# Kernel optimization log

Hardware: AMD Instinct MI355X
Metric: run time of the kernel (lower is better)

Reference implementation:

```python
import jax, jax.numpy as jnp
import numpy as np
from jax import lax

B, N, C_IN, H, W = 256, 64, 3, 8, 8
CH = [32, 64, 128]   # cnn channels per stage
D = 128              # fc / gnn width
OUT = 5
BN_EPS = 1e-5


def setup_inputs() -> dict:
    key = jax.random.key(0)
    ks = jax.random.split(key, 24)
    x = jax.random.normal(ks[0], (B, N, C_IN, H, W), jnp.float32)
    # sparse symmetric communication graph, no self loops (GCNConv adds them)
    a = jax.random.uniform(ks[1], (B, N, N)) < 0.15
    a = jnp.logical_or(a, jnp.swapaxes(a, 1, 2)).astype(jnp.float32)
    gso = a * (1.0 - jnp.eye(N, dtype=jnp.float32))

    def lin(k, o, i):
        return (jax.random.normal(k, (o, i), jnp.float32) / np.sqrt(i)).astype(jnp.float32)

    def conv(k, o, i):
        return (jax.random.normal(k, (o, i, 3, 3), jnp.float32) / np.sqrt(i * 9)).astype(jnp.float32)

    inp = {
        'x': x, 'gso': gso,
        'w_c1': conv(ks[2], CH[0], C_IN), 'b_c1': jnp.zeros((CH[0],), jnp.float32),
        'g_bn1': jnp.ones((CH[0],), jnp.float32), 'be_bn1': jnp.zeros((CH[0],), jnp.float32),
        'w_c2': conv(ks[3], CH[1], CH[0]), 'b_c2': jnp.zeros((CH[1],), jnp.float32),
        'g_bn2': jnp.ones((CH[1],), jnp.float32), 'be_bn2': jnp.zeros((CH[1],), jnp.float32),
        'w_c3': conv(ks[4], CH[2], CH[1]), 'b_c3': jnp.zeros((CH[2],), jnp.float32),
        'g_bn3': jnp.ones((CH[2],), jnp.float32), 'be_bn3': jnp.zeros((CH[2],), jnp.float32),
        'w_fc': lin(ks[5], D, CH[2]), 'b_fc': jnp.zeros((D,), jnp.float32),
        'w_g1': lin(ks[6], D, D), 'b_g1': jnp.zeros((D,), jnp.float32),
        'w_g2': lin(ks[7], D, D), 'b_g2': jnp.zeros((D,), jnp.float32),
        'w_out': lin(ks[8], OUT, D), 'b_out': jnp.zeros((OUT,), jnp.float32),
    }
    return inp


def _cnn_block(h, w, b, g, be):
    h = lax.conv_general_dilated(h, w, (1, 1), 'SAME',
                                 dimension_numbers=('NCHW', 'OIHW', 'NCHW'))
    h = h + b[None, :, None, None]
    # eval-mode BatchNorm2d with running_mean=0, running_var=1
    h = h * (g / jnp.sqrt(1.0 + BN_EPS))[None, :, None, None] + be[None, :, None, None]
    h = jax.nn.relu(h)
    h = lax.reduce_window(h, -jnp.inf, lax.max, (1, 1, 2, 2), (1, 1, 2, 2), 'VALID')
    return h


def _forward(x, gso, w_c1, b_c1, g_bn1, be_bn1, w_c2, b_c2, g_bn2, be_bn2,
             w_c3, b_c3, g_bn3, be_bn3, w_fc, b_fc, w_g1, b_g1, w_g2, b_g2,
             w_out, b_out):
    b, n = x.shape[0], x.shape[1]
    h = x.reshape(b * n, x.shape[2], x.shape[3], x.shape[4])  # vectorize agents
    h = _cnn_block(h, w_c1, b_c1, g_bn1, be_bn1)
    h = _cnn_block(h, w_c2, b_c2, g_bn2, be_bn2)
    h = _cnn_block(h, w_c3, b_c3, g_bn3, be_bn3)          # [B*N, CH2, 1, 1]
    h = h.reshape(b * n, -1)
    h = jax.nn.relu(h @ w_fc.T + b_fc)                    # [B*N, D]
    feat = h.reshape(b, n, -1)
    # GCNConv: add self loops (weight 1), symmetric normalization
    a1 = gso + jnp.eye(n, dtype=gso.dtype)
    dinv = lax.rsqrt(a1.sum(-1))                          # deg >= 1
    ahat = dinv[:, :, None] * a1 * dinv[:, None, :]       # [B, N, N]
    hg = jax.nn.relu(jnp.einsum('bij,bjf->bif', ahat, feat @ w_g1.T) + b_g1)
    hg = jax.nn.relu(jnp.einsum('bij,bjf->bif', ahat, hg @ w_g2.T) + b_g2)
    actions = hg @ w_out.T + b_out                        # [B, N, OUT]
    return actions


def reference(x, gso, w_c1, b_c1, g_bn1, be_bn1, w_c2, b_c2, g_bn2, be_bn2,
              w_c3, b_c3, g_bn3, be_bn3, w_fc, b_fc, w_g1, b_g1, w_g2, b_g2,
              w_out, b_out):
    return _forward(x, gso, w_c1, b_c1, g_bn1, be_bn1, w_c2, b_c2, g_bn2, be_bn2,
                    w_c3, b_c3, g_bn3, be_bn3, w_fc, b_fc, w_g1, b_g1, w_g2, b_g2,
                    w_out, b_out)
```

## Files before the change

kernel.cpp:

```cpp
#include <hip/hip_runtime.h>
#include <math.h>


typedef __attribute__((ext_vector_type(8))) short bf16x8;
typedef __attribute__((ext_vector_type(4))) float f32x4;

__device__ __forceinline__ short f2bf(float f) {
  union { float f; unsigned u; } v; v.f = f;
  unsigned r = v.u + 0x7fffu + ((v.u >> 16) & 1u);
  return (short)(r >> 16);
}
__device__ __forceinline__ float bf2f(unsigned short u) {
  union { unsigned u; float f; } v; v.u = ((unsigned)u) << 16;
  return v.f;
}

__global__ __launch_bounds__(256) void pack_all(
    const float* __restrict__ w_c1, const float* __restrict__ w_c2,
    const float* __restrict__ w_c3, const float* __restrict__ w_fc,
    const float* __restrict__ w_g1, const float* __restrict__ w_g2,
    short* __restrict__ B1, short* __restrict__ B2, short* __restrict__ B3,
    short* __restrict__ Wfc, short* __restrict__ Wg1, short* __restrict__ Wg2) {
  int idx = blockIdx.x * 256 + threadIdx.x;
  if (idx < 2048) {
    int j = idx & 7, lane = (idx >> 3) & 63, f = idx >> 9;
    int nt = f >> 1, ksp = f & 1;
    int col = lane & 15, quad = lane >> 4;
    int k = ksp * 32 + quad * 8 + j;
    int t = k >> 2, ic = k & 3;
    int oc = nt * 16 + col;
    float v = (t < 9 && ic < 3) ? w_c1[(oc * 3 + ic) * 9 + t] : 0.0f;
    B1[idx] = f2bf(v);
  } else if (idx < 20480) {
    int i2 = idx - 2048;
    int j = i2 & 7, lane = (i2 >> 3) & 63, f = i2 >> 9;
    int nt = f / 9, t = f - nt * 9;
    int col = lane & 15, quad = lane >> 4;
    int oc = nt * 16 + col, ic = quad * 8 + j;
    B2[i2] = f2bf(w_c2[(oc * 32 + ic) * 9 + t]);
  } else if (idx < 94208) {
    int i3 = idx - 20480;
    int j = i3 & 7, lane = (i3 >> 3) & 63, f = i3 >> 9;
    int ng = f / 18, ks = f - ng * 18;
    int col = lane & 15, quad = lane >> 4;
    int oc = ng * 16 + col;
    int k = ks * 32 + quad * 8 + j;
    int t = k >> 6, ic = k & 63;
    B3[i3] = f2bf(w_c3[(oc * 64 + ic) * 9 + t]);
  } else if (idx < 110592) {
    int i = idx - 94208; Wfc[i] = f2bf(w_fc[i]);
  } else if (idx < 126976) {
    int i = idx - 110592; Wg1[i] = f2bf(w_g1[i]);
  } else if (idx < 143360) {
    int i = idx - 126976; Wg2[i] = f2bf(w_g2[i]);
  }
}

__global__ __launch_bounds__(256, 2) void conv_all(
    const float* __restrict__ x, const short* __restrict__ B1f,
    const short* __restrict__ B2f, const short* __restrict__ B3f,
    const float* __restrict__ b1, const float* __restrict__ g1,
    const float* __restrict__ e1, const float* __restrict__ b2,
    const float* __restrict__ g2, const float* __restrict__ e2,
    const float* __restrict__ b3, const float* __restrict__ g3,
    const float* __restrict__ e3, short* __restrict__ c3) {
  __shared__ short sFrame[16 * 400];
  __shared__ short sc1[16 * 512];
  __shared__ short sc2[16 * 256];
  const int tid = threadIdx.x;
  const int s0 = blockIdx.x * 16;
  const int lane = tid & 63, w = tid >> 6;
  const int col = lane & 15, quad = lane >> 4;
  const int m = lane & 15;

  for (int i = tid; i < 800; i += 256)
    *(uint4*)(sFrame + i * 8) = (uint4){0, 0, 0, 0};
  __syncthreads();
#pragma unroll
  for (int it = 0; it < 4; ++it) {
    int p = it * 256 + tid;
    int si = p >> 6, pix = p & 63;
    int y = pix >> 3, xx2 = pix & 7;
    const float* xb = x + (s0 + si) * 192 + pix;
    ushort4 o;
    o.x = (unsigned short)f2bf(xb[0]);
    o.y = (unsigned short)f2bf(xb[64]);
    o.z = (unsigned short)f2bf(xb[128]);
    o.w = 0;
    *(ushort4*)(sFrame + si * 400 + ((y + 1) * 10 + xx2 + 1) * 4) = o;
  }
  __syncthreads();

  {
    bf16x8 Bf[2][2];
#pragma unroll
    for (int nt = 0; nt < 2; ++nt)
#pragma unroll
      for (int ks = 0; ks < 2; ++ks)
        Bf[nt][ks] = *(const bf16x8*)(B1f + ((nt * 2 + ks) << 9) + lane * 8);
    float Abn[2], Cbn[2];
#pragma unroll
    for (int nt = 0; nt < 2; ++nt) {
      int oc = nt * 16 + col;
      float a = g1[oc] * rsqrtf(1.0f + 1e-5f);
      Abn[nt] = a;
      Cbn[nt] = fmaf(b1[oc], a, e1[oc]);
    }
    const int t0 = 2 * quad, t1 = t0 + 1;
    const int ky0 = t0 / 3, kx0 = t0 - 3 * (t0 / 3);
    const int ky1 = t1 / 3, kx1 = t1 - 3 * (t1 / 3);
    const int pl = m >> 2, sub = m & 3;
    const int dy = sub >> 1, dx = sub & 1;
    const uint2 z2 = {0u, 0u};
#pragma unroll
    for (int sl = 0; sl < 4; ++sl) {
      const int si = w * 4 + sl;
      const short* xb = sFrame + si * 400;
#pragma unroll
      for (int tile = 0; tile < 4; ++tile) {
        const int pi = tile * 4 + pl;
        const int py = pi >> 2, px = pi & 3;
        const int cy = 2 * py + dy, cx = 2 * px + dx;
        union { bf16x8 v; uint2 u[2]; } a0, a1;
        a0.u[0] = *(const uint2*)(xb + ((cy + ky0) * 10 + cx + kx0) * 4);
        a0.u[1] = *(const uint2*)(xb + ((cy + ky1) * 10 + cx + kx1) * 4);
        uint2 u8 = *(const uint2*)(xb + ((cy + 2) * 10 + cx + 2) * 4);
        a1.u[0] = (quad == 0) ? u8 : z2;
        a1.u[1] = z2;
        f32x4 acc0 = {0, 0, 0, 0}, acc1 = {0, 0, 0, 0};
        acc0 = __builtin_amdgcn_mfma_f32_16x16x32_bf16(a0.v, Bf[0][0], acc0, 0, 0, 0);
        acc0 = __builtin_amdgcn_mfma_f32_16x16x32_bf16(a1.v, Bf[0][1], acc0, 0, 0, 0);
        acc1 = __builtin_amdgcn_mfma_f32_16x16x32_bf16(a0.v, Bf[1][0], acc1, 0, 0, 0);
        acc1 = __builtin_amdgcn_mfma_f32_16x16x32_bf16(a1.v, Bf[1][1], acc1, 0, 0, 0);
        const int piq = tile * 4 + quad;
#pragma unroll
        for (int nt = 0; nt < 2; ++nt) {
          f32x4 acc = nt ? acc1 : acc0;
          float p0 = fmaf(acc[0], Abn[nt], Cbn[nt]);
          float p1 = fmaf(acc[1], Abn[nt], Cbn[nt]);
          float p2 = fmaf(acc[2], Abn[nt], Cbn[nt]);
          float p3 = fmaf(acc[3], Abn[nt], Cbn[nt]);
          float mx = fmaxf(fmaxf(fmaxf(p0, p1), fmaxf(p2, p3)), 0.0f);
          sc1[si * 512 + piq * 32 + nt * 16 + col] = f2bf(mx);
        }
      }
    }
  }
  __syncthreads();

  {
    bf16x8 Bf[4][9];
#pragma unroll
    for (int nt = 0; nt < 4; ++nt)
#pragma unroll
      for (int t = 0; t < 9; ++t)
        Bf[nt][t] = *(const bf16x8*)(B2f + ((nt * 9 + t) << 9) + lane * 8);
    float Abn[4], Cbn[4];
#pragma unroll
    for (int nt = 0; nt < 4; ++nt) {
      int oc = nt * 16 + col;
      float a = g2[oc] * rsqrtf(1.0f + 1e-5f);
      Abn[nt] = a;
      Cbn[nt] = fmaf(b2[oc], a, e2[oc]);
    }
    const int q2 = m >> 2, sub = m & 3;
    const int cy = 2 * (q2 >> 1) + (sub >> 1);
    const int cx = 2 * (q2 & 1) + (sub & 1);
    int off[9];
    bool valid[9];
#pragma unroll
    for (int t = 0; t < 9; ++t) {
      int ky = t / 3, kx = t - 3 * (t / 3);
      int yy = cy + ky - 1, xx = cx + kx - 1;
      valid[t] = ((unsigned)yy < 4u) && ((unsigned)xx < 4u);
      int yc = min(max(yy, 0), 3), xc = min(max(xx, 0), 3);
      off[t] = (yc * 4 + xc) * 32 + quad * 8;
    }
    const bf16x8 zf = {0, 0, 0, 0, 0, 0, 0, 0};
#pragma unroll
    for (int sl = 0; sl < 4; ++sl) {
      const int si = w * 4 + sl;
      const short* ib = sc1 + si * 512;
      f32x4 acc[4];
#pragma unroll
      for (int nt = 0; nt < 4; ++nt) acc[nt] = (f32x4){0, 0, 0, 0};
#pragma unroll
      for (int t = 0; t < 9; ++t) {
        bf16x8 a = *(const bf16x8*)(ib + off[t]);
        if (!valid[t]) a = zf;
#pragma unroll
        for (int nt = 0; nt < 4; ++nt)
          acc[nt] = __builtin_amdgcn_mfma_f32_16x16x32_bf16(a, Bf[nt][t], acc[nt], 0, 0, 0);
      }
#pragma unroll
      for (int nt = 0; nt < 4; ++nt) {
        float p0 = fmaf(acc[nt][0], Abn[nt], Cbn[nt]);
        float p1 = fmaf(acc[nt][1], Abn[nt], Cbn[nt]);
        float p2 = fmaf(acc[nt][2], Abn[nt], Cbn[nt]);
        float p3 = fmaf(acc[nt][3], Abn[nt], Cbn[nt]);
        float mx = fmaxf(fmaxf(fmaxf(p0, p1), fmaxf(p2, p3)), 0.0f);
        sc2[si * 256 + quad * 64 + nt * 16 + col] = f2bf(mx);
      }
    }
  }
  __syncthreads();

  {
    const int cp = m & 3, sl3 = m >> 2;
    const int cy = cp >> 1, cx = cp & 1;
    const short* ib = sc2 + (w * 4 + sl3) * 256;
    bf16x8 A[18];
    const bf16x8 zf = {0, 0, 0, 0, 0, 0, 0, 0};
#pragma unroll
    for (int ks = 0; ks < 18; ++ks) {
      int t = ks >> 1;
      int ky = t / 3, kx = t - 3 * (t / 3);
      int iy = cy + ky - 1, ix = cx + kx - 1;
      bool valid = ((unsigned)iy < 2u) && ((unsigned)ix < 2u);
      int iyc = min(max(iy, 0), 1), ixc = min(max(ix, 0), 1);
      bf16x8 a = *(const bf16x8*)(ib + (iyc * 2 + ixc) * 64 + (ks & 1) * 32 + quad * 8);
      A[ks] = valid ? a : zf;
    }
    f32x4 acc[8];
#pragma unroll
    for (int i = 0; i < 8; ++i) acc[i] = (f32x4){0, 0, 0, 0};
#pragma unroll
    for (int ng = 0; ng < 8; ++ng) {
#pragma unroll
      for (int ks = 0; ks < 18; ++ks) {
        bf16x8 b = *(const bf16x8*)(B3f + (((ng * 18 + ks) << 6) + lane) * 8);
        acc[ng] = __builtin_amdgcn_mfma_f32_16x16x32_bf16(A[ks], b, acc[ng], 0, 0, 0);
      }
    }
    const int sample = s0 + w * 4 + quad;
#pragma unroll
    for (int ng = 0; ng < 8; ++ng) {
      int oc = ng * 16 + col;
      float a = g3[oc] * rsqrtf(1.0f + 1e-5f);
      float cc = fmaf(b3[oc], a, e3[oc]);
      float p0 = fmaf(acc[ng][0], a, cc);
      float p1 = fmaf(acc[ng][1], a, cc);
      float p2 = fmaf(acc[ng][2], a, cc);
      float p3 = fmaf(acc[ng][3], a, cc);
      float mx = fmaxf(fmaxf(fmaxf(p0, p1), fmaxf(p2, p3)), 0.0f);
      c3[sample * 128 + oc] = f2bf(mx);
    }
  }
}

__global__ __launch_bounds__(512) void fused_dense(
    const short* __restrict__ c3, const float* __restrict__ gso,
    const short* __restrict__ Wfc, const short* __restrict__ Wg1,
    const short* __restrict__ Wg2, const float* __restrict__ b_fc,
    const float* __restrict__ b_g1, const float* __restrict__ b_g2,
    const float* __restrict__ w_o, const float* __restrict__ b_o,
    float* __restrict__ out) {
  __shared__ short sAct[64 * 136];
  __shared__ short sT[128 * 72];
  __shared__ short sAhat[64 * 72];
  __shared__ float sDinv[64];
  __shared__ float sWo[640];
  const int tid = threadIdx.x;
  const int b = blockIdx.x;
  float* sG = (float*)sT;
  for (int i = tid; i < 4096; i += 512) sG[i] = gso[b * 4096 + i];
  for (int i = tid; i < 640; i += 512) sWo[i] = w_o[i];
  __syncthreads();
  if (tid < 64) {
    float ssum = 1.0f;
    for (int j = 0; j < 64; ++j) ssum += sG[j * 64 + tid];
    sDinv[tid] = rsqrtf(ssum);
  }
  __syncthreads();
  for (int i = tid; i < 4096; i += 512) {
    int r = i >> 6, c = i & 63;
    float v = sDinv[r] * (sG[i] + (r == c ? 1.0f : 0.0f)) * sDinv[c];
    sAhat[r * 72 + c] = f2bf(v);
  }
  for (int i = tid; i < 1024; i += 512) {
    int r = i >> 4, seg = i & 15;
    *(bf16x8*)(sAct + r * 136 + seg * 8) =
        *(const bf16x8*)(c3 + (b * 64 + r) * 128 + seg * 8);
  }
  __syncthreads();
  const int lane = tid & 63, w8 = tid >> 6;
  const int rg = w8 >> 1, nh = w8 & 1;
  const int col = lane & 15, quad = lane >> 4;
  const int arow = (rg * 16 + col) * 136;
  const int crow0 = (rg * 16 + quad * 4) * 136;
  bf16x8 A[4];
  f32x4 acc[4];

#pragma unroll
  for (int ks = 0; ks < 4; ++ks)
    A[ks] = *(const bf16x8*)(sAct + arow + ks * 32 + quad * 8);
  __syncthreads();
#pragma unroll
  for (int i = 0; i < 4; ++i) acc[i] = (f32x4){0, 0, 0, 0};
#pragma unroll
  for (int ntl = 0; ntl < 4; ++ntl) {
    const int n = (nh * 4 + ntl) * 16 + col;
#pragma unroll
    for (int ks = 0; ks < 4; ++ks) {
      bf16x8 bb = *(const bf16x8*)(Wfc + n * 128 + ks * 32 + quad * 8);
      acc[ntl] = __builtin_amdgcn_mfma_f32_16x16x32_bf16(A[ks], bb, acc[ntl], 0, 0, 0);
    }
  }
#pragma unroll
  for (int ntl = 0; ntl < 4; ++ntl) {
    const int n = (nh * 4 + ntl) * 16 + col;
    const float bv = b_fc[n];
#pragma unroll
    for (int reg = 0; reg < 4; ++reg)
      sAct[crow0 + reg * 136 + n] = f2bf(fmaxf(acc[ntl][reg] + bv, 0.0f));
  }
  __syncthreads();

#pragma unroll
  for (int ks = 0; ks < 4; ++ks)
    A[ks] = *(const bf16x8*)(sAct + arow + ks * 32 + quad * 8);
#pragma unroll
  for (int i = 0; i < 4; ++i) acc[i] = (f32x4){0, 0, 0, 0};
#pragma unroll
  for (int ntl = 0; ntl < 4; ++ntl) {
    const int n = (nh * 4 + ntl) * 16 + col;
#pragma unroll
    for (int ks = 0; ks < 4; ++ks) {
      bf16x8 bb = *(const bf16x8*)(Wg1 + n * 128 + ks * 32 + quad * 8);
      acc[ntl] = __builtin_amdgcn_mfma_f32_16x16x32_bf16(A[ks], bb, acc[ntl], 0, 0, 0);
    }
  }
#pragma unroll
  for (int ntl = 0; ntl < 4; ++ntl) {
    const int n = (nh * 4 + ntl) * 16 + col;
    ushort4 pk;
    pk.x = (unsigned short)f2bf(acc[ntl][0]);
    pk.y = (unsigned short)f2bf(acc[ntl][1]);
    pk.z = (unsigned short)f2bf(acc[ntl][2]);
    pk.w = (unsigned short)f2bf(acc[ntl][3]);
    *(ushort4*)(sT + n * 72 + rg * 16 + quad * 4) = pk;
  }
  __syncthreads();

  bf16x8 Ah[2];
#pragma unroll
  for (int ks = 0; ks < 2; ++ks)
    Ah[ks] = *(const bf16x8*)(sAhat + (rg * 16 + col) * 72 + ks * 32 + quad * 8);
#pragma unroll
  for (int i = 0; i < 4; ++i) acc[i] = (f32x4){0, 0, 0, 0};
#pragma unroll
  for (int ntl = 0; ntl < 4; ++ntl) {
    const int n = (nh * 4 + ntl) * 16 + col;
#pragma unroll
    for (int ks = 0; ks < 2; ++ks) {
      bf16x8 bb = *(const bf16x8*)(sT + n * 72 + ks * 32 + quad * 8);
      acc[ntl] = __builtin_amdgcn_mfma_f32_16x16x32_bf16(Ah[ks], bb, acc[ntl], 0, 0, 0);
    }
  }
#pragma unroll
  for (int ntl = 0; ntl < 4; ++ntl) {
    const int n = (nh * 4 + ntl) * 16 + col;
    const float bv = b_g1[n];
#pragma unroll
    for (int reg = 0; reg < 4; ++reg)
      sAct[crow0 + reg * 136 + n] = f2bf(fmaxf(acc[ntl][reg] + bv, 0.0f));
  }
  __syncthreads();

#pragma unroll
  for (int ks = 0; ks < 4; ++ks)
    A[ks] = *(const bf16x8*)(sAct + arow + ks * 32 + quad * 8);
#pragma unroll
  for (int i = 0; i < 4; ++i) acc[i] = (f32x4){0, 0, 0, 0};
#pragma unroll
  for (int ntl = 0; ntl < 4; ++ntl) {
    const int n = (nh * 4 + ntl) * 16 + col;
#pragma unroll
    for (int ks = 0; ks < 4; ++ks) {
      bf16x8 bb = *(const bf16x8*)(Wg2 + n * 128 + ks * 32 + quad * 8);
      acc[ntl] = __builtin_amdgcn_mfma_f32_16x16x32_bf16(A[ks], bb, acc[ntl], 0, 0, 0);
    }
  }
#pragma unroll
  for (int ntl = 0; ntl < 4; ++ntl) {
    const int n = (nh * 4 + ntl) * 16 + col;
    ushort4 pk;
    pk.x = (unsigned short)f2bf(acc[ntl][0]);
    pk.y = (unsigned short)f2bf(acc[ntl][1]);
    pk.z = (unsigned short)f2bf(acc[ntl][2]);
    pk.w = (unsigned short)f2bf(acc[ntl][3]);
    *(ushort4*)(sT + n * 72 + rg * 16 + quad * 4) = pk;
  }
  __syncthreads();

#pragma unroll
  for (int i = 0; i < 4; ++i) acc[i] = (f32x4){0, 0, 0, 0};
#pragma unroll
  for (int ntl = 0; ntl < 4; ++ntl) {
    const int n = (nh * 4 + ntl) * 16 + col;
#pragma unroll
    for (int ks = 0; ks < 2; ++ks) {
      bf16x8 bb = *(const bf16x8*)(sT + n * 72 + ks * 32 + quad * 8);
      acc[ntl] = __builtin_amdgcn_mfma_f32_16x16x32_bf16(Ah[ks], bb, acc[ntl], 0, 0, 0);
    }
  }
#pragma unroll
  for (int ntl = 0; ntl < 4; ++ntl) {
    const int n = (nh * 4 + ntl) * 16 + col;
    const float bv = b_g2[n];
#pragma unroll
    for (int reg = 0; reg < 4; ++reg)
      sAct[crow0 + reg * 136 + n] = f2bf(fmaxf(acc[ntl][reg] + bv, 0.0f));
  }
  __syncthreads();

  if (tid < 320) {
    const int j = tid / 5, o = tid - 5 * j;
    float a0 = 0.0f;
#pragma unroll
    for (int k8 = 0; k8 < 16; ++k8) {
      union { bf16x8 v; unsigned short u[8]; } h;
      h.v = *(const bf16x8*)(sAct + j * 136 + k8 * 8);
#pragma unroll
      for (int jj = 0; jj < 8; ++jj)
        a0 = fmaf(bf2f(h.u[jj]), sWo[o * 128 + k8 * 8 + jj], a0);
    }
    out[(b * 64 + j) * 5 + o] = a0 + b_o[o];
  }
}

extern "C" void kernel_launch(void* const* d_in, const int* in_sizes, int n_in,
                              void* d_out, int out_size, void* d_ws, size_t ws_size,
                              hipStream_t stream) {
  const float* x    = (const float*)d_in[0];
  const float* gso  = (const float*)d_in[1];
  const float* w_c1 = (const float*)d_in[2];
  const float* b_c1 = (const float*)d_in[3];
  const float* g_b1 = (const float*)d_in[4];
  const float* e_b1 = (const float*)d_in[5];
  const float* w_c2 = (const float*)d_in[6];
  const float* b_c2 = (const float*)d_in[7];
  const float* g_b2 = (const float*)d_in[8];
  const float* e_b2 = (const float*)d_in[9];
  const float* w_c3 = (const float*)d_in[10];
  const float* b_c3 = (const float*)d_in[11];
  const float* g_b3 = (const float*)d_in[12];
  const float* e_b3 = (const float*)d_in[13];
  const float* w_fc = (const float*)d_in[14];
  const float* b_fc = (const float*)d_in[15];
  const float* w_g1 = (const float*)d_in[16];
  const float* b_g1 = (const float*)d_in[17];
  const float* w_g2 = (const float*)d_in[18];
  const float* b_g2 = (const float*)d_in[19];
  const float* w_o  = (const float*)d_in[20];
  const float* b_o  = (const float*)d_in[21];
  float* out = (float*)d_out;
  char* ws = (char*)d_ws;

  short* c3  = (short*)(ws + 0);
  short* B1  = (short*)(ws + 4194304);
  short* B2  = (short*)(ws + 4198400);
  short* B3  = (short*)(ws + 4235264);
  short* Wfc = (short*)(ws + 4382720);
  short* Wg1 = (short*)(ws + 4415488);
  short* Wg2 = (short*)(ws + 4448256);

  pack_all<<<560, 256, 0, stream>>>(w_c1, w_c2, w_c3, w_fc, w_g1, w_g2,
                                    B1, B2, B3, Wfc, Wg1, Wg2);
  conv_all<<<1024, 256, 0, stream>>>(x, B1, B2, B3, b_c1, g_b1, e_b1,
                                     b_c2, g_b2, e_b2, b_c3, g_b3, e_b3, c3);
  fused_dense<<<256, 512, 0, stream>>>(c3, gso, Wfc, Wg1, Wg2, b_fc, b_g1,
                                       b_g2, w_o, b_o, out);
}
```

Baseline: 156.8 us.

## Halve conv block tile and stream weights to raise occupancy

Each conv_all block now processes 8 samples instead of 16, and the grid doubles to 2048 blocks. Conv2 weight fragments are loaded per MFMA instead of being held in registers, and conv3 splits output channel groups across wave pairs rather than one wave per four samples, so A fragments are no longer kept in registers. Together with launch bounds raised to 6 blocks per EU, this cuts register and LDS pressure to increase occupancy. In exchange, weights are re-read from global/L2 memory more often and per-block fixed overhead doubles.

```diff
diff --git a/kernel.cpp b/kernel.cpp
--- a/kernel.cpp
+++ b/kernel.cpp
@@ -56,7 +56,7 @@
   }
 }
 
-__global__ __launch_bounds__(256, 2) void conv_all(
+__global__ __launch_bounds__(256, 6) void conv_all(
     const float* __restrict__ x, const short* __restrict__ B1f,
     const short* __restrict__ B2f, const short* __restrict__ B3f,
     const float* __restrict__ b1, const float* __restrict__ g1,
@@ -64,20 +64,20 @@
     const float* __restrict__ g2, const float* __restrict__ e2,
     const float* __restrict__ b3, const float* __restrict__ g3,
     const float* __restrict__ e3, short* __restrict__ c3) {
-  __shared__ short sFrame[16 * 400];
-  __shared__ short sc1[16 * 512];
-  __shared__ short sc2[16 * 256];
+  __shared__ short sFrame[8 * 400];
+  __shared__ short sc1[8 * 512];
+  __shared__ short sc2[8 * 256];
   const int tid = threadIdx.x;
-  const int s0 = blockIdx.x * 16;
+  const int s0 = blockIdx.x * 8;
   const int lane = tid & 63, w = tid >> 6;
   const int col = lane & 15, quad = lane >> 4;
   const int m = lane & 15;
 
-  for (int i = tid; i < 800; i += 256)
+  for (int i = tid; i < 400; i += 256)
     *(uint4*)(sFrame + i * 8) = (uint4){0, 0, 0, 0};
   __syncthreads();
 #pragma unroll
-  for (int it = 0; it < 4; ++it) {
+  for (int it = 0; it < 2; ++it) {
     int p = it * 256 + tid;
     int si = p >> 6, pix = p & 63;
     int y = pix >> 3, xx2 = pix & 7;
@@ -113,8 +113,8 @@
     const int dy = sub >> 1, dx = sub & 1;
     const uint2 z2 = {0u, 0u};
 #pragma unroll
-    for (int sl = 0; sl < 4; ++sl) {
-      const int si = w * 4 + sl;
+    for (int sl = 0; sl < 2; ++sl) {
+      const int si = w * 2 + sl;
       const short* xb = sFrame + si * 400;
 #pragma unroll
       for (int tile = 0; tile < 4; ++tile) {
@@ -149,12 +149,6 @@
   __syncthreads();
 
   {
-    bf16x8 Bf[4][9];
-#pragma unroll
-    for (int nt = 0; nt < 4; ++nt)
-#pragma unroll
-      for (int t = 0; t < 9; ++t)
-        Bf[nt][t] = *(const bf16x8*)(B2f + ((nt * 9 + t) << 9) + lane * 8);
     float Abn[4], Cbn[4];
 #pragma unroll
     for (int nt = 0; nt < 4; ++nt) {
@@ -178,8 +172,8 @@
     }
     const bf16x8 zf = {0, 0, 0, 0, 0, 0, 0, 0};
 #pragma unroll
-    for (int sl = 0; sl < 4; ++sl) {
-      const int si = w * 4 + sl;
+    for (int sl = 0; sl < 2; ++sl) {
+      const int si = w * 2 + sl;
       const short* ib = sc1 + si * 512;
       f32x4 acc[4];
 #pragma unroll
@@ -189,8 +183,10 @@
         bf16x8 a = *(const bf16x8*)(ib + off[t]);
         if (!valid[t]) a = zf;
 #pragma unroll
-        for (int nt = 0; nt < 4; ++nt)
-          acc[nt] = __builtin_amdgcn_mfma_f32_16x16x32_bf16(a, Bf[nt][t], acc[nt], 0, 0, 0);
+        for (int nt = 0; nt < 4; ++nt) {
+          bf16x8 bb = *(const bf16x8*)(B2f + ((nt * 9 + t) << 9) + lane * 8);
+          acc[nt] = __builtin_amdgcn_mfma_f32_16x16x32_bf16(a, bb, acc[nt], 0, 0, 0);
+        }
       }
 #pragma unroll
       for (int nt = 0; nt < 4; ++nt) {
@@ -206,42 +202,39 @@
   __syncthreads();
 
   {
+    const int sg = w & 1, ngb = (w >> 1) * 4;
     const int cp = m & 3, sl3 = m >> 2;
     const int cy = cp >> 1, cx = cp & 1;
-    const short* ib = sc2 + (w * 4 + sl3) * 256;
-    bf16x8 A[18];
+    const short* ib = sc2 + (sg * 4 + sl3) * 256;
     const bf16x8 zf = {0, 0, 0, 0, 0, 0, 0, 0};
+    f32x4 acc[4];
+#pragma unroll
+    for (int i = 0; i < 4; ++i) acc[i] = (f32x4){0, 0, 0, 0};
 #pragma unroll
     for (int ks = 0; ks < 18; ++ks) {
-      int t = ks >> 1;
-      int ky = t / 3, kx = t - 3 * (t / 3);
-      int iy = cy + ky - 1, ix = cx + kx - 1;
-      bool valid = ((unsigned)iy < 2u) && ((unsigned)ix < 2u);
-      int iyc = min(max(iy, 0), 1), ixc = min(max(ix, 0), 1);
+      const int t = ks >> 1;
+      const int ky = t / 3, kx = t - 3 * (t / 3);
+      const int iy = cy + ky - 1, ix = cx + kx - 1;
+      const bool valid = ((unsigned)iy < 2u) && ((unsigned)ix < 2u);
+      const int iyc = min(max(iy, 0), 1), ixc = min(max(ix, 0), 1);
       bf16x8 a = *(const bf16x8*)(ib + (iyc * 2 + ixc) * 64 + (ks & 1) * 32 + quad * 8);
-      A[ks] = valid ? a : zf;
-    }
-    f32x4 acc[8];
-#pragma unroll
-    for (int i = 0; i < 8; ++i) acc[i] = (f32x4){0, 0, 0, 0};
-#pragma unroll
-    for (int ng = 0; ng < 8; ++ng) {
-#pragma unroll
-      for (int ks = 0; ks < 18; ++ks) {
-        bf16x8 b = *(const bf16x8*)(B3f + (((ng * 18 + ks) << 6) + lane) * 8);
-        acc[ng] = __builtin_amdgcn_mfma_f32_16x16x32_bf16(A[ks], b, acc[ng], 0, 0, 0);
+      if (!valid) a = zf;
+#pragma unroll
+      for (int ngl = 0; ngl < 4; ++ngl) {
+        bf16x8 bb = *(const bf16x8*)(B3f + ((((ngb + ngl) * 18 + ks) << 6) + lane) * 8);
+        acc[ngl] = __builtin_amdgcn_mfma_f32_16x16x32_bf16(a, bb, acc[ngl], 0, 0, 0);
       }
     }
-    const int sample = s0 + w * 4 + quad;
-#pragma unroll
-    for (int ng = 0; ng < 8; ++ng) {
-      int oc = ng * 16 + col;
+    const int sample = s0 + sg * 4 + quad;
+#pragma unroll
+    for (int ngl = 0; ngl < 4; ++ngl) {
+      int oc = (ngb + ngl) * 16 + col;
       float a = g3[oc] * rsqrtf(1.0f + 1e-5f);
       float cc = fmaf(b3[oc], a, e3[oc]);
-      float p0 = fmaf(acc[ng][0], a, cc);
-      float p1 = fmaf(acc[ng][1], a, cc);
-      float p2 = fmaf(acc[ng][2], a, cc);
-      float p3 = fmaf(acc[ng][3], a, cc);
+      float p0 = fmaf(acc[ngl][0], a, cc);
+      float p1 = fmaf(acc[ngl][1], a, cc);
+      float p2 = fmaf(acc[ngl][2], a, cc);
+      float p3 = fmaf(acc[ngl][3], a, cc);
       float mx = fmaxf(fmaxf(fmaxf(p0, p1), fmaxf(p2, p3)), 0.0f);
       c3[sample * 128 + oc] = f2bf(mx);
     }
@@ -467,7 +460,7 @@
 
   pack_all<<<560, 256, 0, stream>>>(w_c1, w_c2, w_c3, w_fc, w_g1, w_g2,
                                     B1, B2, B3, Wfc, Wg1, Wg2);
-  conv_all<<<1024, 256, 0, stream>>>(x, B1, B2, B3, b_c1, g_b1, e_b1,
+  conv_all<<<2048, 256, 0, stream>>>(x, B1, B2, B3, b_c1, g_b1, e_b1,
                                      b_c2, g_b2, e_b2, b_c3, g_b3, e_b3, c3);
   fused_dense<<<256, 512, 0, stream>>>(c3, gso, Wfc, Wg1, Wg2, b_fc, b_g1,
                                        b_g2, w_o, b_o, out);
```

Result: slower. 178.8 us (+14.0%).

## Fuse conv stack and dense/GCN stages into one per-batch kernel

Applied to the files above, without the earlier changes.

Merges the conv kernel and the dense/GCN kernel into a single kernel with one block per graph. Each block loops over four 16-sample chunks of conv work and writes the conv3 features straight into shared memory instead of a global buffer. Shared memory is aliased between the conv and dense phases, and the dense phase is remapped from 8 to 4 waves per block. This removes a kernel launch and the global round trip for conv3 features. The cost is a grid of only 256 blocks of 256 threads, giving far less parallelism for the conv work, which was previously spread across 1024 blocks.

```diff
diff --git a/kernel.cpp b/kernel.cpp
--- a/kernel.cpp
+++ b/kernel.cpp
@@ -56,215 +56,216 @@
   }
 }
 
-__global__ __launch_bounds__(256, 2) void conv_all(
-    const float* __restrict__ x, const short* __restrict__ B1f,
-    const short* __restrict__ B2f, const short* __restrict__ B3f,
+__global__ __launch_bounds__(256) void net_fused(
+    const float* __restrict__ x, const float* __restrict__ gso,
+    const short* __restrict__ B1f, const short* __restrict__ B2f,
+    const short* __restrict__ B3f, const short* __restrict__ Wfc,
+    const short* __restrict__ Wg1, const short* __restrict__ Wg2,
     const float* __restrict__ b1, const float* __restrict__ g1,
     const float* __restrict__ e1, const float* __restrict__ b2,
     const float* __restrict__ g2, const float* __restrict__ e2,
     const float* __restrict__ b3, const float* __restrict__ g3,
-    const float* __restrict__ e3, short* __restrict__ c3) {
-  __shared__ short sFrame[16 * 400];
-  __shared__ short sc1[16 * 512];
-  __shared__ short sc2[16 * 256];
+    const float* __restrict__ e3, const float* __restrict__ b_fc,
+    const float* __restrict__ b_g1, const float* __restrict__ b_g2,
+    const float* __restrict__ w_o, const float* __restrict__ b_o,
+    float* __restrict__ out) {
+  __shared__ short sBuf[18688];
+  __shared__ short sAct[64 * 136];
+  short* sFrame = sBuf;
+  short* sc1 = sBuf + 6400;
+  short* sc2 = sBuf + 14592;
+  short* sT = sBuf;
+  short* sAhat = sBuf + 9216;
+  float* sWo = (float*)(sBuf + 13824);
+  float* sDinv = (float*)(sBuf + 15104);
   const int tid = threadIdx.x;
-  const int s0 = blockIdx.x * 16;
+  const int b = blockIdx.x;
   const int lane = tid & 63, w = tid >> 6;
   const int col = lane & 15, quad = lane >> 4;
   const int m = lane & 15;
 
-  for (int i = tid; i < 800; i += 256)
-    *(uint4*)(sFrame + i * 8) = (uint4){0, 0, 0, 0};
-  __syncthreads();
-#pragma unroll
-  for (int it = 0; it < 4; ++it) {
-    int p = it * 256 + tid;
-    int si = p >> 6, pix = p & 63;
-    int y = pix >> 3, xx2 = pix & 7;
-    const float* xb = x + (s0 + si) * 192 + pix;
-    ushort4 o;
-    o.x = (unsigned short)f2bf(xb[0]);
-    o.y = (unsigned short)f2bf(xb[64]);
-    o.z = (unsigned short)f2bf(xb[128]);
-    o.w = 0;
-    *(ushort4*)(sFrame + si * 400 + ((y + 1) * 10 + xx2 + 1) * 4) = o;
-  }
-  __syncthreads();
-
-  {
-    bf16x8 Bf[2][2];
-#pragma unroll
-    for (int nt = 0; nt < 2; ++nt)
-#pragma unroll
-      for (int ks = 0; ks < 2; ++ks)
-        Bf[nt][ks] = *(const bf16x8*)(B1f + ((nt * 2 + ks) << 9) + lane * 8);
-    float Abn[2], Cbn[2];
-#pragma unroll
-    for (int nt = 0; nt < 2; ++nt) {
-      int oc = nt * 16 + col;
-      float a = g1[oc] * rsqrtf(1.0f + 1e-5f);
-      Abn[nt] = a;
-      Cbn[nt] = fmaf(b1[oc], a, e1[oc]);
-    }
-    const int t0 = 2 * quad, t1 = t0 + 1;
-    const int ky0 = t0 / 3, kx0 = t0 - 3 * (t0 / 3);
-    const int ky1 = t1 / 3, kx1 = t1 - 3 * (t1 / 3);
-    const int pl = m >> 2, sub = m & 3;
-    const int dy = sub >> 1, dx = sub & 1;
-    const uint2 z2 = {0u, 0u};
-#pragma unroll
-    for (int sl = 0; sl < 4; ++sl) {
-      const int si = w * 4 + sl;
-      const short* xb = sFrame + si * 400;
-#pragma unroll
-      for (int tile = 0; tile < 4; ++tile) {
-        const int pi = tile * 4 + pl;
-        const int py = pi >> 2, px = pi & 3;
-        const int cy = 2 * py + dy, cx = 2 * px + dx;
-        union { bf16x8 v; uint2 u[2]; } a0, a1;
-        a0.u[0] = *(const uint2*)(xb + ((cy + ky0) * 10 + cx + kx0) * 4);
-        a0.u[1] = *(const uint2*)(xb + ((cy + ky1) * 10 + cx + kx1) * 4);
-        uint2 u8 = *(const uint2*)(xb + ((cy + 2) * 10 + cx + 2) * 4);
-        a1.u[0] = (quad == 0) ? u8 : z2;
-        a1.u[1] = z2;
-        f32x4 acc0 = {0, 0, 0, 0}, acc1 = {0, 0, 0, 0};
-        acc0 = __builtin_amdgcn_mfma_f32_16x16x32_bf16(a0.v, Bf[0][0], acc0, 0, 0, 0);
-        acc0 = __builtin_amdgcn_mfma_f32_16x16x32_bf16(a1.v, Bf[0][1], acc0, 0, 0, 0);
-        acc1 = __builtin_amdgcn_mfma_f32_16x16x32_bf16(a0.v, Bf[1][0], acc1, 0, 0, 0);
-        acc1 = __builtin_amdgcn_mfma_f32_16x16x32_bf16(a1.v, Bf[1][1], acc1, 0, 0, 0);
-        const int piq = tile * 4 + quad;
-#pragma unroll
-        for (int nt = 0; nt < 2; ++nt) {
-          f32x4 acc = nt ? acc1 : acc0;
-          float p0 = fmaf(acc[0], Abn[nt], Cbn[nt]);
-          float p1 = fmaf(acc[1], Abn[nt], Cbn[nt]);
-          float p2 = fmaf(acc[2], Abn[nt], Cbn[nt]);
-          float p3 = fmaf(acc[3], Abn[nt], Cbn[nt]);
+#pragma unroll 1
+  for (int chunk = 0; chunk < 4; ++chunk) {
+    const int s0 = b * 64 + chunk * 16;
+    for (int i = tid; i < 800; i += 256)
+      *(uint4*)(sFrame + i * 8) = (uint4){0, 0, 0, 0};
+    __syncthreads();
+#pragma unroll
+    for (int it = 0; it < 4; ++it) {
+      int p = it * 256 + tid;
+      int si = p >> 6, pix = p & 63;
+      int y = pix >> 3, xx2 = pix & 7;
+      const float* xb = x + (s0 + si) * 192 + pix;
+      ushort4 o;
+      o.x = (unsigned short)f2bf(xb[0]);
+      o.y = (unsigned short)f2bf(xb[64]);
+      o.z = (unsigned short)f2bf(xb[128]);
+      o.w = 0;
+      *(ushort4*)(sFrame + si * 400 + ((y + 1) * 10 + xx2 + 1) * 4) = o;
+    }
+    __syncthreads();
+
+    {
+      bf16x8 Bf[2][2];
+#pragma unroll
+      for (int nt = 0; nt < 2; ++nt)
+#pragma unroll
+        for (int ks = 0; ks < 2; ++ks)
+          Bf[nt][ks] = *(const bf16x8*)(B1f + ((nt * 2 + ks) << 9) + lane * 8);
+      float Abn[2], Cbn[2];
+#pragma unroll
+      for (int nt = 0; nt < 2; ++nt) {
+        int oc = nt * 16 + col;
+        float a = g1[oc] * rsqrtf(1.0f + 1e-5f);
+        Abn[nt] = a;
+        Cbn[nt] = fmaf(b1[oc], a, e1[oc]);
+      }
+      const int t0 = 2 * quad, t1 = t0 + 1;
+      const int ky0 = t0 / 3, kx0 = t0 - 3 * (t0 / 3);
+      const int ky1 = t1 / 3, kx1 = t1 - 3 * (t1 / 3);
+      const int pl = m >> 2, sub = m & 3;
+      const int dy = sub >> 1, dx = sub & 1;
+      const uint2 z2 = {0u, 0u};
+#pragma unroll
+      for (int sl = 0; sl < 4; ++sl) {
+        const int si = w * 4 + sl;
+        const short* xb = sFrame + si * 400;
+#pragma unroll
+        for (int tile = 0; tile < 4; ++tile) {
+          const int pi = tile * 4 + pl;
+          const int py = pi >> 2, px = pi & 3;
+          const int cy = 2 * py + dy, cx = 2 * px + dx;
+          union { bf16x8 v; uint2 u[2]; } a0, a1;
+          a0.u[0] = *(const uint2*)(xb + ((cy + ky0) * 10 + cx + kx0) * 4);
+          a0.u[1] = *(const uint2*)(xb + ((cy + ky1) * 10 + cx + kx1) * 4);
+          uint2 u8 = *(const uint2*)(xb + ((cy + 2) * 10 + cx + 2) * 4);
+          a1.u[0] = (quad == 0) ? u8 : z2;
+          a1.u[1] = z2;
+          f32x4 acc0 = {0, 0, 0, 0}, acc1 = {0, 0, 0, 0};
+          acc0 = __builtin_amdgcn_mfma_f32_16x16x32_bf16(a0.v, Bf[0][0], acc0, 0, 0, 0);
+          acc0 = __builtin_amdgcn_mfma_f32_16x16x32_bf16(a1.v, Bf[0][1], acc0, 0, 0, 0);
+          acc1 = __builtin_amdgcn_mfma_f32_16x16x32_bf16(a0.v, Bf[1][0], acc1, 0, 0, 0);
+          acc1 = __builtin_amdgcn_mfma_f32_16x16x32_bf16(a1.v, Bf[1][1], acc1, 0, 0, 0);
+          const int piq = tile * 4 + quad;
+#pragma unroll
+          for (int nt = 0; nt < 2; ++nt) {
+            f32x4 acc = nt ? acc1 : acc0;
+            float p0 = fmaf(acc[0], Abn[nt], Cbn[nt]);
+            float p1 = fmaf(acc[1], Abn[nt], Cbn[nt]);
+            float p2 = fmaf(acc[2], Abn[nt], Cbn[nt]);
+            float p3 = fmaf(acc[3], Abn[nt], Cbn[nt]);
+            float mx = fmaxf(fmaxf(fmaxf(p0, p1), fmaxf(p2, p3)), 0.0f);
+            sc1[si * 512 + piq * 32 + nt * 16 + col] = f2bf(mx);
+          }
+        }
+      }
+    }
+    __syncthreads();
+
+    {
+      bf16x8 Bf[4][9];
+#pragma unroll
+      for (int nt = 0; nt < 4; ++nt)
+#pragma unroll
+        for (int t = 0; t < 9; ++t)
+          Bf[nt][t] = *(const bf16x8*)(B2f + ((nt * 9 + t) << 9) + lane * 8);
+      float Abn[4], Cbn[4];
+#pragma unroll
+      for (int nt = 0; nt < 4; ++nt) {
+        int oc = nt * 16 + col;
+        float a = g2[oc] * rsqrtf(1.0f + 1e-5f);
+        Abn[nt] = a;
+        Cbn[nt] = fmaf(b2[oc], a, e2[oc]);
+      }
+      const int q2 = m >> 2, sub = m & 3;
+      const int cy = 2 * (q2 >> 1) + (sub >> 1);
+      const int cx = 2 * (q2 & 1) + (sub & 1);
+      int off[9];
+      bool valid[9];
+#pragma unroll
+      for (int t = 0; t < 9; ++t) {
+        int ky = t / 3, kx = t - 3 * (t / 3);
+        int yy = cy + ky - 1, xx = cx + kx - 1;
+        valid[t] = ((unsigned)yy < 4u) && ((unsigned)xx < 4u);
+        int yc = min(max(yy, 0), 3), xc = min(max(xx, 0), 3);
+        off[t] = (yc * 4 + xc) * 32 + quad * 8;
+      }
+      const bf16x8 zf = {0, 0, 0, 0, 0, 0, 0, 0};
+#pragma unroll
+      for (int sl = 0; sl < 4; ++sl) {
+        const int si = w * 4 + sl;
+        const short* ib = sc1 + si * 512;
+        f32x4 acc[4];
+#pragma unroll
+        for (int nt = 0; nt < 4; ++nt) acc[nt] = (f32x4){0, 0, 0, 0};
+#pragma unroll
+        for (int t = 0; t < 9; ++t) {
+          bf16x8 a = *(const bf16x8*)(ib + off[t]);
+          if (!valid[t]) a = zf;
+#pragma unroll
+          for (int nt = 0; nt < 4; ++nt)
+            acc[nt] = __builtin_amdgcn_mfma_f32_16x16x32_bf16(a, Bf[nt][t], acc[nt], 0, 0, 0);
+        }
+#pragma unroll
+        for (int nt = 0; nt < 4; ++nt) {
+          float p0 = fmaf(acc[nt][0], Abn[nt], Cbn[nt]);
+          float p1 = fmaf(acc[nt][1], Abn[nt], Cbn[nt]);
+          float p2 = fmaf(acc[nt][2], Abn[nt], Cbn[nt]);
+          float p3 = fmaf(acc[nt][3], Abn[nt], Cbn[nt]);
           float mx = fmaxf(fmaxf(fmaxf(p0, p1), fmaxf(p2, p3)), 0.0f);
-          sc1[si * 512 + piq * 32 + nt * 16 + col] = f2bf(mx);
+          sc2[si * 256 + quad * 64 + nt * 16 + col] = f2bf(mx);
         }
       }
     }
-  }
-  __syncthreads();
-
-  {
-    bf16x8 Bf[4][9];
-#pragma unroll
-    for (int nt = 0; nt < 4; ++nt)
-#pragma unroll
-      for (int t = 0; t < 9; ++t)
-        Bf[nt][t] = *(const bf16x8*)(B2f + ((nt * 9 + t) << 9) + lane * 8);
-    float Abn[4], Cbn[4];
-#pragma unroll
-    for (int nt = 0; nt < 4; ++nt) {
-      int oc = nt * 16 + col;
-      float a = g2[oc] * rsqrtf(1.0f + 1e-5f);
-      Abn[nt] = a;
-      Cbn[nt] = fmaf(b2[oc], a, e2[oc]);
-    }
-    const int q2 = m >> 2, sub = m & 3;
-    const int cy = 2 * (q2 >> 1) + (sub >> 1);
-    const int cx = 2 * (q2 & 1) + (sub & 1);
-    int off[9];
-    bool valid[9];
-#pragma unroll
-    for (int t = 0; t < 9; ++t) {
-      int ky = t / 3, kx = t - 3 * (t / 3);
-      int yy = cy + ky - 1, xx = cx + kx - 1;
-      valid[t] = ((unsigned)yy < 4u) && ((unsigned)xx < 4u);
-      int yc = min(max(yy, 0), 3), xc = min(max(xx, 0), 3);
-      off[t] = (yc * 4 + xc) * 32 + quad * 8;
-    }
-    const bf16x8 zf = {0, 0, 0, 0, 0, 0, 0, 0};
-#pragma unroll
-    for (int sl = 0; sl < 4; ++sl) {
-      const int si = w * 4 + sl;
-      const short* ib = sc1 + si * 512;
-      f32x4 acc[4];
-#pragma unroll
-      for (int nt = 0; nt < 4; ++nt) acc[nt] = (f32x4){0, 0, 0, 0};
-#pragma unroll
-      for (int t = 0; t < 9; ++t) {
-        bf16x8 a = *(const bf16x8*)(ib + off[t]);
-        if (!valid[t]) a = zf;
-#pragma unroll
-        for (int nt = 0; nt < 4; ++nt)
-          acc[nt] = __builtin_amdgcn_mfma_f32_16x16x32_bf16(a, Bf[nt][t], acc[nt], 0, 0, 0);
-      }
-#pragma unroll
-      for (int nt = 0; nt < 4; ++nt) {
-        float p0 = fmaf(acc[nt][0], Abn[nt], Cbn[nt]);
-        float p1 = fmaf(acc[nt][1], Abn[nt], Cbn[nt]);
-        float p2 = fmaf(acc[nt][2], Abn[nt], Cbn[nt]);
-        float p3 = fmaf(acc[nt][3], Abn[nt], Cbn[nt]);
+    __syncthreads();
+
+    {
+      const int cp = m & 3, sl3 = m >> 2;
+      const int cy = cp >> 1, cx = cp & 1;
+      const short* ib = sc2 + (w * 4 + sl3) * 256;
+      bf16x8 A[18];
+      const bf16x8 zf = {0, 0, 0, 0, 0, 0, 0, 0};
+#pragma unroll
+      for (int ks = 0; ks < 18; ++ks) {
+        int t = ks >> 1;
+        int ky = t / 3, kx = t - 3 * (t / 3);
+        int iy = cy + ky - 1, ix = cx + kx - 1;
+        bool valid = ((unsigned)iy < 2u) && ((unsigned)ix < 2u);
+        int iyc = min(max(iy, 0), 1), ixc = min(max(ix, 0), 1);
+        bf16x8 a = *(const bf16x8*)(ib + (iyc * 2 + ixc) * 64 + (ks & 1) * 32 + quad * 8);
+        A[ks] = valid ? a : zf;
+      }
+      f32x4 acc[8];
+#pragma unroll
+      for (int i = 0; i < 8; ++i) acc[i] = (f32x4){0, 0, 0, 0};
+#pragma unroll
+      for (int ng = 0; ng < 8; ++ng) {
+#pragma unroll
+        for (int ks = 0; ks < 18; ++ks) {
+          bf16x8 bb = *(const bf16x8*)(B3f + (((ng * 18 + ks) << 6) + lane) * 8);
+          acc[ng] = __builtin_amdgcn_mfma_f32_16x16x32_bf16(A[ks], bb, acc[ng], 0, 0, 0);
+        }
+      }
+      const int arow = (chunk * 16 + w * 4 + quad) * 136;
+#pragma unroll
+      for (int ng = 0; ng < 8; ++ng) {
+        int oc = ng * 16 + col;
+        float a = g3[oc] * rsqrtf(1.0f + 1e-5f);
+        float cc = fmaf(b3[oc], a, e3[oc]);
+        float p0 = fmaf(acc[ng][0], a, cc);
+        float p1 = fmaf(acc[ng][1], a, cc);
+        float p2 = fmaf(acc[ng][2], a, cc);
+        float p3 = fmaf(acc[ng][3], a, cc);
         float mx = fmaxf(fmaxf(fmaxf(p0, p1), fmaxf(p2, p3)), 0.0f);
-        sc2[si * 256 + quad * 64 + nt * 16 + col] = f2bf(mx);
-      }
-    }
-  }
-  __syncthreads();
-
-  {
-    const int cp = m & 3, sl3 = m >> 2;
-    const int cy = cp >> 1, cx = cp & 1;
-    const short* ib = sc2 + (w * 4 + sl3) * 256;
-    bf16x8 A[18];
-    const bf16x8 zf = {0, 0, 0, 0, 0, 0, 0, 0};
-#pragma unroll
-    for (int ks = 0; ks < 18; ++ks) {
-      int t = ks >> 1;
-      int ky = t / 3, kx = t - 3 * (t / 3);
-      int iy = cy + ky - 1, ix = cx + kx - 1;
-      bool valid = ((unsigned)iy < 2u) && ((unsigned)ix < 2u);
-      int iyc = min(max(iy, 0), 1), ixc = min(max(ix, 0), 1);
-      bf16x8 a = *(const bf16x8*)(ib + (iyc * 2 + ixc) * 64 + (ks & 1) * 32 + quad * 8);
-      A[ks] = valid ? a : zf;
-    }
-    f32x4 acc[8];
-#pragma unroll
-    for (int i = 0; i < 8; ++i) acc[i] = (f32x4){0, 0, 0, 0};
-#pragma unroll
-    for (int ng = 0; ng < 8; ++ng) {
-#pragma unroll
-      for (int ks = 0; ks < 18; ++ks) {
-        bf16x8 b = *(const bf16x8*)(B3f + (((ng * 18 + ks) << 6) + lane) * 8);
-        acc[ng] = __builtin_amdgcn_mfma_f32_16x16x32_bf16(A[ks], b, acc[ng], 0, 0, 0);
-      }
-    }
-    const int sample = s0 + w * 4 + quad;
-#pragma unroll
-    for (int ng = 0; ng < 8; ++ng) {
-      int oc = ng * 16 + col;
-      float a = g3[oc] * rsqrtf(1.0f + 1e-5f);
-      float cc = fmaf(b3[oc], a, e3[oc]);
-      float p0 = fmaf(acc[ng][0], a, cc);
-      float p1 = fmaf(acc[ng][1], a, cc);
-      float p2 = fmaf(acc[ng][2], a, cc);
-      float p3 = fmaf(acc[ng][3], a, cc);
-      float mx = fmaxf(fmaxf(fmaxf(p0, p1), fmaxf(p2, p3)), 0.0f);
-      c3[sample * 128 + oc] = f2bf(mx);
-    }
-  }
-}
-
-__global__ __launch_bounds__(512) void fused_dense(
-    const short* __restrict__ c3, const float* __restrict__ gso,
-    const short* __restrict__ Wfc, const short* __restrict__ Wg1,
-    const short* __restrict__ Wg2, const float* __restrict__ b_fc,
-    const float* __restrict__ b_g1, const float* __restrict__ b_g2,
-    const float* __restrict__ w_o, const float* __restrict__ b_o,
-    float* __restrict__ out) {
-  __shared__ short sAct[64 * 136];
-  __shared__ short sT[128 * 72];
-  __shared__ short sAhat[64 * 72];
-  __shared__ float sDinv[64];
-  __shared__ float sWo[640];
-  const int tid = threadIdx.x;
-  const int b = blockIdx.x;
+        sAct[arow + oc] = f2bf(mx);
+      }
+    }
+    __syncthreads();
+  }
+
   float* sG = (float*)sT;
-  for (int i = tid; i < 4096; i += 512) sG[i] = gso[b * 4096 + i];
-  for (int i = tid; i < 640; i += 512) sWo[i] = w_o[i];
+  for (int i = tid; i < 4096; i += 256) sG[i] = gso[b * 4096 + i];
+  for (int i = tid; i < 640; i += 256) sWo[i] = w_o[i];
   __syncthreads();
   if (tid < 64) {
     float ssum = 1.0f;
@@ -272,150 +273,144 @@
     sDinv[tid] = rsqrtf(ssum);
   }
   __syncthreads();
-  for (int i = tid; i < 4096; i += 512) {
+  for (int i = tid; i < 4096; i += 256) {
     int r = i >> 6, c = i & 63;
     float v = sDinv[r] * (sG[i] + (r == c ? 1.0f : 0.0f)) * sDinv[c];
     sAhat[r * 72 + c] = f2bf(v);
   }
-  for (int i = tid; i < 1024; i += 512) {
-    int r = i >> 4, seg = i & 15;
-    *(bf16x8*)(sAct + r * 136 + seg * 8) =
-        *(const bf16x8*)(c3 + (b * 64 + r) * 128 + seg * 8);
-  }
-  __syncthreads();
-  const int lane = tid & 63, w8 = tid >> 6;
-  const int rg = w8 >> 1, nh = w8 & 1;
-  const int col = lane & 15, quad = lane >> 4;
-  const int arow = (rg * 16 + col) * 136;
-  const int crow0 = (rg * 16 + quad * 4) * 136;
+  __syncthreads();
+  const int arow = (w * 16 + col) * 136;
+  const int crow0 = (w * 16 + quad * 4) * 136;
   bf16x8 A[4];
-  f32x4 acc[4];
+  f32x4 acc[8];
 
 #pragma unroll
   for (int ks = 0; ks < 4; ++ks)
     A[ks] = *(const bf16x8*)(sAct + arow + ks * 32 + quad * 8);
   __syncthreads();
 #pragma unroll
-  for (int i = 0; i < 4; ++i) acc[i] = (f32x4){0, 0, 0, 0};
-#pragma unroll
-  for (int ntl = 0; ntl < 4; ++ntl) {
-    const int n = (nh * 4 + ntl) * 16 + col;
+  for (int i = 0; i < 8; ++i) acc[i] = (f32x4){0, 0, 0, 0};
+#pragma unroll
+  for (int nt = 0; nt < 8; ++nt) {
+    const int n = nt * 16 + col;
 #pragma unroll
     for (int ks = 0; ks < 4; ++ks) {
       bf16x8 bb = *(const bf16x8*)(Wfc + n * 128 + ks * 32 + quad * 8);
-      acc[ntl] = __builtin_amdgcn_mfma_f32_16x16x32_bf16(A[ks], bb, acc[ntl], 0, 0, 0);
-    }
-  }
-#pragma unroll
-  for (int ntl = 0; ntl < 4; ++ntl) {
-    const int n = (nh * 4 + ntl) * 16 + col;
+      acc[nt] = __builtin_amdgcn_mfma_f32_16x16x32_bf16(A[ks], bb, acc[nt], 0, 0, 0);
+    }
+  }
+#pragma unroll
+  for (int nt = 0; nt < 8; ++nt) {
+    const int n = nt * 16 + col;
     const float bv = b_fc[n];
 #pragma unroll
     for (int reg = 0; reg < 4; ++reg)
-      sAct[crow0 + reg * 136 + n] = f2bf(fmaxf(acc[ntl][reg] + bv, 0.0f));
+      sAct[crow0 + reg * 136 + n] = f2bf(fmaxf(acc[nt][reg] + bv, 0.0f));
   }
   __syncthreads();
 
 #pragma unroll
   for (int ks = 0; ks < 4; ++ks)
     A[ks] = *(const bf16x8*)(sAct + arow + ks * 32 + quad * 8);
-#pragma unroll
-  for (int i = 0; i < 4; ++i) acc[i] = (f32x4){0, 0, 0, 0};
-#pragma unroll
-  for (int ntl = 0; ntl < 4; ++ntl) {
-    const int n = (nh * 4 + ntl) * 16 + col;
+  __syncthreads();
+#pragma unroll
+  for (int i = 0; i < 8; ++i) acc[i] = (f32x4){0, 0, 0, 0};
+#pragma unroll
+  for (int nt = 0; nt < 8; ++nt) {
+    const int n = nt * 16 + col;
 #pragma unroll
     for (int ks = 0; ks < 4; ++ks) {
       bf16x8 bb = *(const bf16x8*)(Wg1 + n * 128 + ks * 32 + quad * 8);
-      acc[ntl] = __builtin_amdgcn_mfma_f32_16x16x32_bf16(A[ks], bb, acc[ntl], 0, 0, 0);
-    }
-  }
-#pragma unroll
-  for (int ntl = 0; ntl < 4; ++ntl) {
-    const int n = (nh * 4 + ntl) * 16 + col;
+      acc[nt] = __builtin_amdgcn_mfma_f32_16x16x32_bf16(A[ks], bb, acc[nt], 0, 0, 0);
+    }
+  }
+#pragma unroll
+  for (int nt = 0; nt < 8; ++nt) {
+    const int n = nt * 16 + col;
     ushort4 pk;
-    pk.x = (unsigned short)f2bf(acc[ntl][0]);
-    pk.y = (unsigned short)f2bf(acc[ntl][1]);
-    pk.z = (unsigned short)f2bf(acc[ntl][2]);
-    pk.w = (unsigned short)f2bf(acc[ntl][3]);
-    *(ushort4*)(sT + n * 72 + rg * 16 + quad * 4) = pk;
+    pk.x = (unsigned short)f2bf(acc[nt][0]);
+    pk.y = (unsigned short)f2bf(acc[nt][1]);
+    pk.z = (unsigned short)f2bf(acc[nt][2]);
+    pk.w = (unsigned short)f2bf(acc[nt][3]);
+    *(ushort4*)(sT + n * 72 + w * 16 + quad * 4) = pk;
   }
   __syncthreads();
 
   bf16x8 Ah[2];
 #pragma unroll
   for (int ks = 0; ks < 2; ++ks)
-    Ah[ks] = *(const bf16x8*)(sAhat + (rg * 16 + col) * 72 + ks * 32 + quad * 8);
-#pragma unroll
-  for (int i = 0; i < 4; ++i) acc[i] = (f32x4){0, 0, 0, 0};
-#pragma unroll
-  for (int ntl = 0; ntl < 4; ++ntl) {
-    const int n = (nh * 4 + ntl) * 16 + col;
+    Ah[ks] = *(const bf16x8*)(sAhat + (w * 16 + col) * 72 + ks * 32 + quad * 8);
+#pragma unroll
+  for (int i = 0; i < 8; ++i) acc[i] = (f32x4){0, 0, 0, 0};
+#pragma unroll
+  for (int nt = 0; nt < 8; ++nt) {
+    const int n = nt * 16 + col;
 #pragma unroll
     for (int ks = 0; ks < 2; ++ks) {
       bf16x8 bb = *(const bf16x8*)(sT + n * 72 + ks * 32 + quad * 8);
-      acc[ntl] = __builtin_amdgcn_mfma_f32_16x16x32_bf16(Ah[ks], bb, acc[ntl], 0, 0, 0);
-    }
-  }
-#pragma unroll
-  for (int ntl = 0; ntl < 4; ++ntl) {
-    const int n = (nh * 4 + ntl) * 16 + col;
+      acc[nt] = __builtin_amdgcn_mfma_f32_16x16x32_bf16(Ah[ks], bb, acc[nt], 0, 0, 0);
+    }
+  }
+#pragma unroll
+  for (int nt = 0; nt < 8; ++nt) {
+    const int n = nt * 16 + col;
     const float bv = b_g1[n];
 #pragma unroll
     for (int reg = 0; reg < 4; ++reg)
-      sAct[crow0 + reg * 136 + n] = f2bf(fmaxf(acc[ntl][reg] + bv, 0.0f));
+      sAct[crow0 + reg * 136 + n] = f2bf(fmaxf(acc[nt][reg] + bv, 0.0f));
   }
   __syncthreads();
 
 #pragma unroll
   for (int ks = 0; ks < 4; ++ks)
     A[ks] = *(const bf16x8*)(sAct + arow + ks * 32 + quad * 8);
-#pragma unroll
-  for (int i = 0; i < 4; ++i) acc[i] = (f32x4){0, 0, 0, 0};
-#pragma unroll
-  for (int ntl = 0; ntl < 4; ++ntl) {
-    const int n = (nh * 4 + ntl) * 16 + col;
+  __syncthreads();
+#pragma unroll
+  for (int i = 0; i < 8; ++i) acc[i] = (f32x4){0, 0, 0, 0};
+#pragma unroll
+  for (int nt = 0; nt < 8; ++nt) {
+    const int n = nt * 16 + col;
 #pragma unroll
     for (int ks = 0; ks < 4; ++ks) {
       bf16x8 bb = *(const bf16x8*)(Wg2 + n * 128 + ks * 32 + quad * 8);
-      acc[ntl] = __builtin_amdgcn_mfma_f32_16x16x32_bf16(A[ks], bb, acc[ntl], 0, 0, 0);
-    }
-  }
-#pragma unroll
-  for (int ntl = 0; ntl < 4; ++ntl) {
-    const int n = (nh * 4 + ntl) * 16 + col;
+      acc[nt] = __builtin_amdgcn_mfma_f32_16x16x32_bf16(A[ks], bb, acc[nt], 0, 0, 0);
+    }
+  }
+#pragma unroll
+  for (int nt = 0; nt < 8; ++nt) {
+    const int n = nt * 16 + col;
     ushort4 pk;
-    pk.x = (unsigned short)f2bf(acc[ntl][0]);
-    pk.y = (unsigned short)f2bf(acc[ntl][1]);
-    pk.z = (unsigned short)f2bf(acc[ntl][2]);
-    pk.w = (unsigned short)f2bf(acc[ntl][3]);
-    *(ushort4*)(sT + n * 72 + rg * 16 + quad * 4) = pk;
-  }
-  __syncthreads();
-
-#pragma unroll
-  for (int i = 0; i < 4; ++i) acc[i] = (f32x4){0, 0, 0, 0};
-#pragma unroll
-  for (int ntl = 0; ntl < 4; ++ntl) {
-    const int n = (nh * 4 + ntl) * 16 + col;
+    pk.x = (unsigned short)f2bf(acc[nt][0]);
+    pk.y = (unsigned short)f2bf(acc[nt][1]);
+    pk.z = (unsigned short)f2bf(acc[nt][2]);
+    pk.w = (unsigned short)f2bf(acc[nt][3]);
+    *(ushort4*)(sT + n * 72 + w * 16 + quad * 4) = pk;
+  }
+  __syncthreads();
+
+#pragma unroll
+  for (int i = 0; i < 8; ++i) acc[i] = (f32x4){0, 0, 0, 0};
+#pragma unroll
+  for (int nt = 0; nt < 8; ++nt) {
+    const int n = nt * 16 + col;
 #pragma unroll
     for (int ks = 0; ks < 2; ++ks) {
       bf16x8 bb = *(const bf16x8*)(sT + n * 72 + ks * 32 + quad * 8);
-      acc[ntl] = __builtin_amdgcn_mfma_f32_16x16x32_bf16(Ah[ks], bb, acc[ntl], 0, 0, 0);
-    }
-  }
-#pragma unroll
-  for (int ntl = 0; ntl < 4; ++ntl) {
-    const int n = (nh * 4 + ntl) * 16 + col;
+      acc[nt] = __builtin_amdgcn_mfma_f32_16x16x32_bf16(Ah[ks], bb, acc[nt], 0, 0, 0);
+    }
+  }
+#pragma unroll
+  for (int nt = 0; nt < 8; ++nt) {
+    const int n = nt * 16 + col;
     const float bv = b_g2[n];
 #pragma unroll
     for (int reg = 0; reg < 4; ++reg)
-      sAct[crow0 + reg * 136 + n] = f2bf(fmaxf(acc[ntl][reg] + bv, 0.0f));
-  }
-  __syncthreads();
-
-  if (tid < 320) {
-    const int j = tid / 5, o = tid - 5 * j;
+      sAct[crow0 + reg * 136 + n] = f2bf(fmaxf(acc[nt][reg] + bv, 0.0f));
+  }
+  __syncthreads();
+
+  {
+    const int j = tid >> 2, o = tid & 3;
     float a0 = 0.0f;
 #pragma unroll
     for (int k8 = 0; k8 < 16; ++k8) {
@@ -426,6 +421,18 @@
         a0 = fmaf(bf2f(h.u[jj]), sWo[o * 128 + k8 * 8 + jj], a0);
     }
     out[(b * 64 + j) * 5 + o] = a0 + b_o[o];
+    if (tid < 64) {
+      float a4 = 0.0f;
+#pragma unroll
+      for (int k8 = 0; k8 < 16; ++k8) {
+        union { bf16x8 v; unsigned short u[8]; } h;
+        h.v = *(const bf16x8*)(sAct + tid * 136 + k8 * 8);
+#pragma unroll
+        for (int jj = 0; jj < 8; ++jj)
+          a4 = fmaf(bf2f(h.u[jj]), sWo[512 + k8 * 8 + jj], a4);
+      }
+      out[(b * 64 + tid) * 5 + 4] = a4 + b_o[4];
+    }
   }
 }
 
@@ -457,18 +464,17 @@
   float* out = (float*)d_out;
   char* ws = (char*)d_ws;
 
-  short* c3  = (short*)(ws + 0);
-  short* B1  = (short*)(ws + 4194304);
-  short* B2  = (short*)(ws + 4198400);
-  short* B3  = (short*)(ws + 4235264);
-  short* Wfc = (short*)(ws + 4382720);
-  short* Wg1 = (short*)(ws + 4415488);
-  short* Wg2 = (short*)(ws + 4448256);
+  short* B1  = (short*)(ws + 0);
+  short* B2  = (short*)(ws + 4096);
+  short* B3  = (short*)(ws + 40960);
+  short* Wfc = (short*)(ws + 188416);
+  short* Wg1 = (short*)(ws + 221184);
+  short* Wg2 = (short*)(ws + 253952);
 
   pack_all<<<560, 256, 0, stream>>>(w_c1, w_c2, w_c3, w_fc, w_g1, w_g2,
                                     B1, B2, B3, Wfc, Wg1, Wg2);
-  conv_all<<<1024, 256, 0, stream>>>(x, B1, B2, B3, b_c1, g_b1, e_b1,
-                                     b_c2, g_b2, e_b2, b_c3, g_b3, e_b3, c3);
-  fused_dense<<<256, 512, 0, stream>>>(c3, gso, Wfc, Wg1, Wg2, b_fc, b_g1,
-                                       b_g2, w_o, b_o, out);
+  net_fused<<<256, 256, 0, stream>>>(x, gso, B1, B2, B3, Wfc, Wg1, Wg2,
+                                     b_c1, g_b1, e_b1, b_c2, g_b2, e_b2,
+                                     b_c3, g_b3, e_b3, b_fc, b_g1, b_g2,
+                                     w_o, b_o, out);
 }
```

Result: slower. 333.1 us (+112.4%).
